# Performance work log

Measured on AMD Instinct MI355X. Metric: run time of the kernel, lower is better.

Reference implementation:

```python
import jax, jax.numpy as jnp
from jax import lax
import numpy as np

H = 51  # hidden size hardcoded in the module


def setup_inputs() -> dict:
    key = jax.random.key(0)
    ks = jax.random.split(key, 12)
    B, T = 4096, 256
    s_in = 1.0 / np.sqrt(H)
    inp = {
        "input": jax.random.normal(ks[0], (B, T), dtype=jnp.float32),
        # LSTMCell 1: input dim 1 -> hidden 51 (gates stacked i,f,g,o)
        "W_ih1": jax.random.uniform(ks[1], (4 * H, 1), jnp.float32, -s_in, s_in),
        "W_hh1": jax.random.uniform(ks[2], (4 * H, H), jnp.float32, -s_in, s_in),
        "b_ih1": jax.random.uniform(ks[3], (4 * H,), jnp.float32, -s_in, s_in),
        "b_hh1": jax.random.uniform(ks[4], (4 * H,), jnp.float32, -s_in, s_in),
        # LSTMCell 2: hidden 51 -> hidden 51
        "W_ih2": jax.random.uniform(ks[5], (4 * H, H), jnp.float32, -s_in, s_in),
        "W_hh2": jax.random.uniform(ks[6], (4 * H, H), jnp.float32, -s_in, s_in),
        "b_ih2": jax.random.uniform(ks[7], (4 * H,), jnp.float32, -s_in, s_in),
        "b_hh2": jax.random.uniform(ks[8], (4 * H,), jnp.float32, -s_in, s_in),
        # Linear head 51 -> 1
        "W_lin": jax.random.uniform(ks[9], (1, H), jnp.float32, -s_in, s_in),
        "b_lin": jax.random.uniform(ks[10], (1,), jnp.float32, -s_in, s_in),
    }
    return inp


def _lstm_cell(x_t, h, c, W_ih, W_hh, b_ih, b_hh):
    # PyTorch LSTMCell: gates = x W_ih^T + b_ih + h W_hh^T + b_hh, order i,f,g,o
    g = x_t @ W_ih.T + b_ih + h @ W_hh.T + b_hh  # [B, 4H]
    i, f, gg, o = jnp.split(g, 4, axis=-1)
    c_new = jax.nn.sigmoid(f) * c + jax.nn.sigmoid(i) * jnp.tanh(gg)
    h_new = jax.nn.sigmoid(o) * jnp.tanh(c_new)
    return h_new, c_new


def reference(input, W_ih1, W_hh1, b_ih1, b_hh1, W_ih2, W_hh2, b_ih2, b_hh2, W_lin, b_lin):
    B = input.shape[0]
    xs = input.T[:, :, None]  # [T, B, 1] -- one scalar feature per timestep

    def step(carry, x_t):
        h1, c1, h2, c2 = carry
        h1, c1 = _lstm_cell(x_t, h1, c1, W_ih1, W_hh1, b_ih1, b_hh1)
        h2, c2 = _lstm_cell(h1, h2, c2, W_ih2, W_hh2, b_ih2, b_hh2)
        out = h2 @ W_lin.T + b_lin  # [B, 1]
        return (h1, c1, h2, c2), out

    z = jnp.zeros((B, H), dtype=input.dtype)
    _, outs = lax.scan(step, (z, z, z, z), xs)  # outs: [T, B, 1]
    # torch.stack(outputs, 1).squeeze(2) -> [B, T]
    return outs[:, :, 0].T
```

## Files before the change

kernel.cpp:

```cpp
#include <hip/hip_runtime.h>

#define HH 51
#define TT 256
#define NB 16
#define L2E 1.442695041f

typedef __attribute__((ext_vector_type(8))) _Float16 half8;
typedef __attribute__((ext_vector_type(4))) float   floatx4;

#define MFMA16F(A,B,C) __builtin_amdgcn_mfma_f32_16x16x32_f16((A),(B),(C),0,0,0)

__device__ __forceinline__ float rcp_fast(float x) { return __builtin_amdgcn_rcpf(x); }
#if __has_builtin(__builtin_amdgcn_exp2f)
__device__ __forceinline__ float exp2_fast(float x) { return __builtin_amdgcn_exp2f(x); }
#else
__device__ __forceinline__ float exp2_fast(float x) { return __expf(0.69314718056f * x); }
#endif
__device__ __forceinline__ unsigned short f2h_bits(float v) {
    return __builtin_bit_cast(unsigned short, (_Float16)v);
}

__global__ void lstm_prep(const float* __restrict__ Whh1, const float* __restrict__ Wih1,
                          const float* __restrict__ bih1, const float* __restrict__ bhh1,
                          const float* __restrict__ Wih2, const float* __restrict__ Whh2,
                          const float* __restrict__ bih2, const float* __restrict__ bhh2,
                          const float* __restrict__ Wlin, const float* __restrict__ blin,
                          uint4* __restrict__ frags) {
    int tid = blockIdx.x * blockDim.x + threadIdx.x;
    if (tid >= 196 * 64) return;
    int f = tid >> 6, lane = tid & 63;
    int n = lane & 15, qq = lane >> 4;
    int hl, s, tau, cell;
    if (f < 64)       { cell = 1; int r = f;       hl = r & 1; r >>= 1; s = r & 1; tau = r >> 1; }
    else if (f < 192) { cell = 2; int r = f - 64;  hl = r & 1; r >>= 1; s = r & 3; tau = r >> 2; }
    else              { cell = 3; int r = f - 192; hl = r & 1; s = r >> 1; tau = 0; }
    int g = tau >> 2, U = tau & 3, u = U * 16 + n;
    float sc = (cell == 3) ? 1.0f : ((g == 2) ? 2.0f * L2E : L2E);
    unsigned int dw[4];
    for (int d = 0; d < 4; d++) {
        unsigned int packed = 0;
        for (int e = 0; e < 2; e++) {
            int jj = d * 2 + e;
            int k = s * 32 + qq * 8 + jj;
            float val = 0.f;
            if (cell == 1) {
                if (u < HH) {
                    if (k < HH)       val = Whh1[(g * HH + u) * HH + k];
                    else if (k == 51) val = bih1[g * HH + u] + bhh1[g * HH + u];
                    else              val = Wih1[g * HH + u];
                }
            } else if (cell == 2) {
                if (u < HH) {
                    if (k < 64) {
                        if (k < HH)       val = Wih2[(g * HH + u) * HH + k];
                        else if (k == 51) val = bih2[g * HH + u] + bhh2[g * HH + u];
                    } else {
                        int k2 = k - 64;
                        if (k2 < HH) val = Whh2[(g * HH + u) * HH + k2];
                    }
                }
            } else {
                if (n == 0) {
                    if (k < HH)       val = Wlin[k];
                    else if (k == 51) val = blin[0];
                }
            }
            val *= sc;
            _Float16 hi = (_Float16)val;
            unsigned short bits;
            if (hl) { float lo = val - (float)hi; bits = f2h_bits(lo); }
            else    { bits = __builtin_bit_cast(unsigned short, hi); }
            packed |= ((unsigned int)bits) << (16 * e);
        }
        dw[d] = packed;
    }
    frags[f * 64 + lane] = make_uint4(dw[0], dw[1], dw[2], dw[3]);
}

__launch_bounds__(512, 2)
__global__ void lstm_main(const float* __restrict__ input,
                          const uint4* __restrict__ frags,
                          float* __restrict__ out) {
    __shared__ __align__(16) unsigned int h1[2][16][36];
    __shared__ __align__(16) unsigned int h2[2][16][36];
    __shared__ __align__(16) float xb[(TT + 1) * 16];

    const int tid  = threadIdx.x;
    const int lane = tid & 63;
    const int w    = tid >> 6;
    const int l15  = lane & 15;
    const int q    = lane >> 4;
    const int b0g  = blockIdx.x * NB;
    const bool c2w = (w < 4);
    const int U    = c2w ? w : (w - 4);
    const int uc   = U * 16 + l15;
    const bool uok = (uc < HH);

    for (int i = tid; i < 2 * 16 * 36; i += 512) {
        ((unsigned*)h1)[i] = 0; ((unsigned*)h2)[i] = 0;
    }
    for (int c = 0; c < 2; c++) {
        int flat = tid + c * 512;
        int b = flat >> 6, t0 = (flat & 63) * 4;
        float4 v = *(const float4*)&input[(size_t)(b0g + b) * TT + t0];
        xb[(t0 + 0) * 16 + b] = v.x; xb[(t0 + 1) * 16 + b] = v.y;
        xb[(t0 + 2) * 16 + b] = v.z; xb[(t0 + 3) * 16 + b] = v.w;
    }
    if (tid < 16) xb[TT * 16 + tid] = 0.f;
    __syncthreads();
    if (tid < 16) {
        int b = tid;
        int wi51 = ((25 + 4 * (b >> 1)) & 31) * 2 + 1;
        int wi52 = ((26 + 4 * (b >> 1)) & 31) * 2 + 0;
        int wi53 = ((26 + 4 * (b >> 1)) & 31) * 2 + 1;
        ((unsigned short*)&h1[1][b][0])[wi51] = 0x3C00;
        float x0 = input[(size_t)(b0g + b) * TT];
        _Float16 xh = (_Float16)x0;
        ((unsigned short*)&h1[1][b][0])[wi52] = __builtin_bit_cast(unsigned short, xh);
        ((unsigned short*)&h1[1][b][0])[wi53] = f2h_bits(x0 - (float)xh);
    }

    half8 fr[32];
    if (c2w) {
#pragma unroll
        for (int g = 0; g < 4; g++) {
            int tau = g * 4 + U;
#pragma unroll
            for (int s = 0; s < 4; s++) {
                fr[g * 8 + s * 2 + 0] = __builtin_bit_cast(half8, frags[(64 + (tau * 4 + s) * 2 + 0) * 64 + lane]);
                fr[g * 8 + s * 2 + 1] = __builtin_bit_cast(half8, frags[(64 + (tau * 4 + s) * 2 + 1) * 64 + lane]);
            }
        }
    } else {
#pragma unroll
        for (int g = 0; g < 4; g++) {
            int tau = g * 4 + U;
#pragma unroll
            for (int s = 0; s < 2; s++) {
                fr[g * 4 + s * 2 + 0] = __builtin_bit_cast(half8, frags[((tau * 2 + s) * 2 + 0) * 64 + lane]);
                fr[g * 4 + s * 2 + 1] = __builtin_bit_cast(half8, frags[((tau * 2 + s) * 2 + 1) * 64 + lane]);
            }
        }
#pragma unroll
        for (int s = 0; s < 2; s++) {
            fr[16 + s * 2 + 0] = __builtin_bit_cast(half8, frags[(192 + s * 2 + 0) * 64 + lane]);
            fr[16 + s * 2 + 1] = __builtin_bit_cast(half8, frags[(192 + s * 2 + 1) * 64 + lane]);
        }
    }
    floatx4 zacc = {0.f, 0.f, 0.f, 0.f};
    float cst[4] = {0.f, 0.f, 0.f, 0.f};
    const int baseA = (q * 4 + 4 * (l15 >> 1)) & 31;
    const int baseB = (baseA + 16) & 31;

    __syncthreads();

#define GTAIL(DG, FG, SGN)                                                      \
    _Pragma("unroll")                                                           \
    for (int r = 0; r < 4; r++) {                                               \
        float e = exp2_fast(SGN (DG)[r]);                                       \
        (FG)[r] = rcp_fast(1.0f + e);                                           \
    }

#define STEP(IT, P)                                                             \
    do {                                                                        \
        if (c2w) {                                                              \
            if ((IT) >= 1 && (IT) <= TT) {               \
                half8 a0 = *(const half8*)&h1[1 - (P)][l15][baseA];             \
                half8 a1 = *(const half8*)&h1[1 - (P)][l15][baseB];             \
                half8 a2 = *(const half8*)&h2[(P)][l15][baseA];                 \
                half8 a3 = *(const half8*)&h2[(P)][l15][baseB];                 \
                floatx4 d0, d1, d2, d3;                                         \
                d0 = MFMA16F(a0, fr[0],  zacc); d0 = MFMA16F(a0, fr[1],  d0);   \
                d1 = MFMA16F(a0, fr[8],  zacc); d1 = MFMA16F(a0, fr[9],  d1);   \
                d2 = MFMA16F(a0, fr[16], zacc); d2 = MFMA16F(a0, fr[17], d2);   \
                d3 = MFMA16F(a0, fr[24], zacc); d3 = MFMA16F(a0, fr[25], d3);   \
                d0 = MFMA16F(a1, fr[2],  d0);   d0 = MFMA16F(a1, fr[3],  d0);   \
                d1 = MFMA16F(a1, fr[10], d1);   d1 = MFMA16F(a1, fr[11], d1);   \
                d2 = MFMA16F(a1, fr[18], d2);   d2 = MFMA16F(a1, fr[19], d2);   \
                d3 = MFMA16F(a1, fr[26], d3);   d3 = MFMA16F(a1, fr[27], d3);   \
                d0 = MFMA16F(a2, fr[4],  d0);   d0 = MFMA16F(a2, fr[5],  d0);   \
                d1 = MFMA16F(a2, fr[12], d1);   d1 = MFMA16F(a2, fr[13], d1);   \
                d2 = MFMA16F(a2, fr[20], d2);   d2 = MFMA16F(a2, fr[21], d2);   \
                d3 = MFMA16F(a2, fr[28], d3);   d3 = MFMA16F(a2, fr[29], d3);   \
                d0 = MFMA16F(a3, fr[6],  d0);   d0 = MFMA16F(a3, fr[7],  d0);   \
                d1 = MFMA16F(a3, fr[14], d1);   d1 = MFMA16F(a3, fr[15], d1);   \
                d2 = MFMA16F(a3, fr[22], d2);   d2 = MFMA16F(a3, fr[23], d2);   \
                d3 = MFMA16F(a3, fr[30], d3);   d3 = MFMA16F(a3, fr[31], d3);   \
                floatx4 f0, f1, f2, f3;                                         \
                GTAIL(d0, f0, -) GTAIL(d1, f1, -) GTAIL(d2, f2, +) GTAIL(d3, f3, -) \
                _Pragma("unroll")                                               \
                for (int r = 0; r < 4; r++) {                                   \
                    float tgs = fmaf(-4.0f * L2E, f2[r], 2.0f * L2E);           \
                    float cn  = fmaf(f1[r], cst[r], f0[r] * tgs);               \
                    cst[r] = cn;                                                \
                    float th = fmaf(-2.0f, rcp_fast(1.0f + exp2_fast(cn)), 1.0f); \
                    float hv = f3[r] * th;                                      \
                    hv = uok ? hv : (uc == 51 ? 1.0f : 0.f);                    \
                    int bb = q * 4 + r;                                         \
                    int wi = (((uc >> 1) + 4 * (bb >> 1)) & 31) * 2 + (uc & 1); \
                    ((unsigned short*)&h2[1 - (P)][bb][0])[wi] = f2h_bits(hv);  \
                }                                                               \
            }                                                                   \
        } else {                                                                \
            if ((IT) <= TT - 1) {                          \
                float4 xn = {0.f, 0.f, 0.f, 0.f};                               \
                if (uc >= HH) xn = *(const float4*)&xb[((IT) + 1) * 16 + q * 4]; \
                half8 a0 = *(const half8*)&h1[1 - (P)][l15][baseA];             \
                half8 a1 = *(const half8*)&h1[1 - (P)][l15][baseB];             \
                floatx4 d0, d1, d2, d3;                                         \
                d0 = MFMA16F(a0, fr[0],  zacc); d0 = MFMA16F(a0, fr[1],  d0);   \
                d1 = MFMA16F(a0, fr[4],  zacc); d1 = MFMA16F(a0, fr[5],  d1);   \
                d2 = MFMA16F(a0, fr[8],  zacc); d2 = MFMA16F(a0, fr[9],  d2);   \
                d3 = MFMA16F(a0, fr[12], zacc); d3 = MFMA16F(a0, fr[13], d3);   \
                d0 = MFMA16F(a1, fr[2],  d0);   d0 = MFMA16F(a1, fr[3],  d0);   \
                d1 = MFMA16F(a1, fr[6],  d1);   d1 = MFMA16F(a1, fr[7],  d1);   \
                d2 = MFMA16F(a1, fr[10], d2);   d2 = MFMA16F(a1, fr[11], d2);   \
                d3 = MFMA16F(a1, fr[14], d3);   d3 = MFMA16F(a1, fr[15], d3);   \
                floatx4 f0, f1, f2, f3;                                         \
                GTAIL(d0, f0, -) GTAIL(d1, f1, -) GTAIL(d2, f2, +) GTAIL(d3, f3, -) \
                _Pragma("unroll")                                               \
                for (int r = 0; r < 4; r++) {                                   \
                    float tgs = fmaf(-4.0f * L2E, f2[r], 2.0f * L2E);           \
                    float cn  = fmaf(f1[r], cst[r], f0[r] * tgs);               \
                    cst[r] = cn;                                                \
                    float th = fmaf(-2.0f, rcp_fast(1.0f + exp2_fast(cn)), 1.0f); \
                    float hv = f3[r] * th;                                      \
                    hv = uok ? hv                                               \
                             : (uc == 51 ? 1.0f                                 \
                             : (uc == 52 ? xn[r]                                \
                             : (uc == 53 ? xn[r] - (float)(_Float16)xn[r] : 0.f))); \
                    int bb = q * 4 + r;                                         \
                    int wi = (((uc >> 1) + 4 * (bb >> 1)) & 31) * 2 + (uc & 1); \
                    ((unsigned short*)&h1[(P)][bb][0])[wi] = f2h_bits(hv);      \
                }                                                               \
            }                                                                   \
            if ((IT) >= 2 && (w - 4) == ((IT) & 3)) {         \
                half8 a2 = *(const half8*)&h2[(P)][l15][baseA];                 \
                half8 a3 = *(const half8*)&h2[(P)][l15][baseB];                 \
                floatx4 ho;                                                     \
                ho = MFMA16F(a2, fr[16], zacc); ho = MFMA16F(a2, fr[17], ho);   \
                ho = MFMA16F(a3, fr[18], ho);   ho = MFMA16F(a3, fr[19], ho);   \
                if (l15 == 0) {                                                 \
                    _Pragma("unroll")                                           \
                    for (int r = 0; r < 4; r++)                                 \
                        out[(size_t)(b0g + q * 4 + r) * TT + ((IT) - 2)] = ho[r]; \
                }                                                               \
            }                                                                   \
        }                                                                       \
        __syncthreads();                                                        \
    } while (0)

    for (int itp = 0; itp < TT + 2; itp += 2) {
        STEP(itp, 0);
        STEP(itp + 1, 1);
    }
#undef STEP
#undef GTAIL
}

extern "C" void kernel_launch(void* const* d_in, const int* in_sizes, int n_in,
                              void* d_out, int out_size, void* d_ws, size_t ws_size,
                              hipStream_t stream) {
    const float* input = (const float*)d_in[0];
    const float* Wih1  = (const float*)d_in[1];
    const float* Whh1  = (const float*)d_in[2];
    const float* bih1  = (const float*)d_in[3];
    const float* bhh1  = (const float*)d_in[4];
    const float* Wih2  = (const float*)d_in[5];
    const float* Whh2  = (const float*)d_in[6];
    const float* bih2  = (const float*)d_in[7];
    const float* bhh2  = (const float*)d_in[8];
    const float* Wlin  = (const float*)d_in[9];
    const float* blin  = (const float*)d_in[10];

    uint4* frags = (uint4*)d_ws;
    int B = in_sizes[0] / TT;

    lstm_prep<<<49, 256, 0, stream>>>(Whh1, Wih1, bih1, bhh1, Wih2, Whh2,
                                      bih2, bhh2, Wlin, blin, frags);
    lstm_main<<<B / NB, 512, 0, stream>>>(input, frags, (float*)d_out);
}
```

Before: 377.2 us.

## Merge both LSTM cells into each wave and halve batch per block

Each wave now computes both layer-1 and layer-2 gates for its hidden-unit slice, instead of splitting the cells across separate 4-wave groups. Blocks drop to 256 threads and 8 batch rows, so twice as many blocks launch. The linear-head fragments are reloaded from global memory on each output step instead of being held in registers. The intent is to cut per-block wave count and spread work over more blocks. In exchange, the two cells now run one after the other inside each wave, half of each 16-row MFMA tile is idle, and register pressure rises from holding both weight sets.

```diff
diff --git a/kernel.cpp b/kernel.cpp
--- a/kernel.cpp
+++ b/kernel.cpp
@@ -2,7 +2,7 @@
 
 #define HH 51
 #define TT 256
-#define NB 16
+#define NB 8
 #define L2E 1.442695041f
 
 typedef __attribute__((ext_vector_type(8))) _Float16 half8;
@@ -77,13 +77,13 @@
     frags[f * 64 + lane] = make_uint4(dw[0], dw[1], dw[2], dw[3]);
 }
 
-__launch_bounds__(512, 2)
+__launch_bounds__(256, 2)
 __global__ void lstm_main(const float* __restrict__ input,
                           const uint4* __restrict__ frags,
                           float* __restrict__ out) {
     __shared__ __align__(16) unsigned int h1[2][16][36];
     __shared__ __align__(16) unsigned int h2[2][16][36];
-    __shared__ __align__(16) float xb[(TT + 1) * 16];
+    __shared__ __align__(16) float xb[(TT + 1) * NB];
 
     const int tid  = threadIdx.x;
     const int lane = tid & 63;
@@ -91,24 +91,22 @@
     const int l15  = lane & 15;
     const int q    = lane >> 4;
     const int b0g  = blockIdx.x * NB;
-    const bool c2w = (w < 4);
-    const int U    = c2w ? w : (w - 4);
-    const int uc   = U * 16 + l15;
+    const int uc   = w * 16 + l15;
     const bool uok = (uc < HH);
 
-    for (int i = tid; i < 2 * 16 * 36; i += 512) {
+    for (int i = tid; i < 2 * 16 * 36; i += 256) {
         ((unsigned*)h1)[i] = 0; ((unsigned*)h2)[i] = 0;
     }
     for (int c = 0; c < 2; c++) {
-        int flat = tid + c * 512;
+        int flat = tid + c * 256;
         int b = flat >> 6, t0 = (flat & 63) * 4;
         float4 v = *(const float4*)&input[(size_t)(b0g + b) * TT + t0];
-        xb[(t0 + 0) * 16 + b] = v.x; xb[(t0 + 1) * 16 + b] = v.y;
-        xb[(t0 + 2) * 16 + b] = v.z; xb[(t0 + 3) * 16 + b] = v.w;
-    }
-    if (tid < 16) xb[TT * 16 + tid] = 0.f;
+        xb[(t0 + 0) * NB + b] = v.x; xb[(t0 + 1) * NB + b] = v.y;
+        xb[(t0 + 2) * NB + b] = v.z; xb[(t0 + 3) * NB + b] = v.w;
+    }
+    if (tid < NB) xb[TT * NB + tid] = 0.f;
     __syncthreads();
-    if (tid < 16) {
+    if (tid < NB) {
         int b = tid;
         int wi51 = ((25 + 4 * (b >> 1)) & 31) * 2 + 1;
         int wi52 = ((26 + 4 * (b >> 1)) & 31) * 2 + 0;
@@ -120,35 +118,24 @@
         ((unsigned short*)&h1[1][b][0])[wi53] = f2h_bits(x0 - (float)xh);
     }
 
-    half8 fr[32];
-    if (c2w) {
+    half8 fr1[16], fr2[32];
 #pragma unroll
-        for (int g = 0; g < 4; g++) {
-            int tau = g * 4 + U;
+    for (int g = 0; g < 4; g++) {
+        int tau = g * 4 + w;
 #pragma unroll
-            for (int s = 0; s < 4; s++) {
-                fr[g * 8 + s * 2 + 0] = __builtin_bit_cast(half8, frags[(64 + (tau * 4 + s) * 2 + 0) * 64 + lane]);
-                fr[g * 8 + s * 2 + 1] = __builtin_bit_cast(half8, frags[(64 + (tau * 4 + s) * 2 + 1) * 64 + lane]);
-            }
-        }
-    } else {
-#pragma unroll
-        for (int g = 0; g < 4; g++) {
-            int tau = g * 4 + U;
-#pragma unroll
-            for (int s = 0; s < 2; s++) {
-                fr[g * 4 + s * 2 + 0] = __builtin_bit_cast(half8, frags[((tau * 2 + s) * 2 + 0) * 64 + lane]);
-                fr[g * 4 + s * 2 + 1] = __builtin_bit_cast(half8, frags[((tau * 2 + s) * 2 + 1) * 64 + lane]);
-            }
+        for (int s = 0; s < 2; s++) {
+            fr1[g * 4 + s * 2 + 0] = __builtin_bit_cast(half8, frags[((tau * 2 + s) * 2 + 0) * 64 + lane]);
+            fr1[g * 4 + s * 2 + 1] = __builtin_bit_cast(half8, frags[((tau * 2 + s) * 2 + 1) * 64 + lane]);
         }
 #pragma unroll
-        for (int s = 0; s < 2; s++) {
-            fr[16 + s * 2 + 0] = __builtin_bit_cast(half8, frags[(192 + s * 2 + 0) * 64 + lane]);
-            fr[16 + s * 2 + 1] = __builtin_bit_cast(half8, frags[(192 + s * 2 + 1) * 64 + lane]);
+        for (int s = 0; s < 4; s++) {
+            fr2[g * 8 + s * 2 + 0] = __builtin_bit_cast(half8, frags[(64 + (tau * 4 + s) * 2 + 0) * 64 + lane]);
+            fr2[g * 8 + s * 2 + 1] = __builtin_bit_cast(half8, frags[(64 + (tau * 4 + s) * 2 + 1) * 64 + lane]);
         }
     }
     floatx4 zacc = {0.f, 0.f, 0.f, 0.f};
-    float cst[4] = {0.f, 0.f, 0.f, 0.f};
+    float cst1[4] = {0.f, 0.f, 0.f, 0.f};
+    float cst2[4] = {0.f, 0.f, 0.f, 0.f};
     const int baseA = (q * 4 + 4 * (l15 >> 1)) & 31;
     const int baseB = (baseA + 16) & 31;
 
@@ -163,87 +150,91 @@
 
 #define STEP(IT, P)                                                             \
     do {                                                                        \
-        if (c2w) {                                                              \
-            if ((IT) >= 1 && (IT) <= TT) {               \
-                half8 a0 = *(const half8*)&h1[1 - (P)][l15][baseA];             \
-                half8 a1 = *(const half8*)&h1[1 - (P)][l15][baseB];             \
-                half8 a2 = *(const half8*)&h2[(P)][l15][baseA];                 \
-                half8 a3 = *(const half8*)&h2[(P)][l15][baseB];                 \
-                floatx4 d0, d1, d2, d3;                                         \
-                d0 = MFMA16F(a0, fr[0],  zacc); d0 = MFMA16F(a0, fr[1],  d0);   \
-                d1 = MFMA16F(a0, fr[8],  zacc); d1 = MFMA16F(a0, fr[9],  d1);   \
-                d2 = MFMA16F(a0, fr[16], zacc); d2 = MFMA16F(a0, fr[17], d2);   \
-                d3 = MFMA16F(a0, fr[24], zacc); d3 = MFMA16F(a0, fr[25], d3);   \
-                d0 = MFMA16F(a1, fr[2],  d0);   d0 = MFMA16F(a1, fr[3],  d0);   \
-                d1 = MFMA16F(a1, fr[10], d1);   d1 = MFMA16F(a1, fr[11], d1);   \
-                d2 = MFMA16F(a1, fr[18], d2);   d2 = MFMA16F(a1, fr[19], d2);   \
-                d3 = MFMA16F(a1, fr[26], d3);   d3 = MFMA16F(a1, fr[27], d3);   \
-                d0 = MFMA16F(a2, fr[4],  d0);   d0 = MFMA16F(a2, fr[5],  d0);   \
-                d1 = MFMA16F(a2, fr[12], d1);   d1 = MFMA16F(a2, fr[13], d1);   \
-                d2 = MFMA16F(a2, fr[20], d2);   d2 = MFMA16F(a2, fr[21], d2);   \
-                d3 = MFMA16F(a2, fr[28], d3);   d3 = MFMA16F(a2, fr[29], d3);   \
-                d0 = MFMA16F(a3, fr[6],  d0);   d0 = MFMA16F(a3, fr[7],  d0);   \
-                d1 = MFMA16F(a3, fr[14], d1);   d1 = MFMA16F(a3, fr[15], d1);   \
-                d2 = MFMA16F(a3, fr[22], d2);   d2 = MFMA16F(a3, fr[23], d2);   \
-                d3 = MFMA16F(a3, fr[30], d3);   d3 = MFMA16F(a3, fr[31], d3);   \
-                floatx4 f0, f1, f2, f3;                                         \
-                GTAIL(d0, f0, -) GTAIL(d1, f1, -) GTAIL(d2, f2, +) GTAIL(d3, f3, -) \
+        half8 a0 = *(const half8*)&h1[1 - (P)][l15][baseA];       \
+        half8 a1 = *(const half8*)&h1[1 - (P)][l15][baseB];                     \
+        half8 a2 = *(const half8*)&h2[(P)][l15][baseA];           \
+        half8 a3 = *(const half8*)&h2[(P)][l15][baseB];                         \
+          \
+        if ((IT) >= 2 && (((IT) & 3) == w)) {                                   \
+            half8 hf0 = __builtin_bit_cast(half8, frags[(192 + 0) * 64 + lane]);\
+            half8 hf1 = __builtin_bit_cast(half8, frags[(192 + 1) * 64 + lane]);\
+            half8 hf2 = __builtin_bit_cast(half8, frags[(192 + 2) * 64 + lane]);\
+            half8 hf3 = __builtin_bit_cast(half8, frags[(192 + 3) * 64 + lane]);\
+            floatx4 ho;                                                         \
+            ho = MFMA16F(a2, hf0, zacc); ho = MFMA16F(a2, hf1, ho);             \
+            ho = MFMA16F(a3, hf2, ho);   ho = MFMA16F(a3, hf3, ho);             \
+            if (l15 == 0 && q < 2) {                                            \
                 _Pragma("unroll")                                               \
-                for (int r = 0; r < 4; r++) {                                   \
-                    float tgs = fmaf(-4.0f * L2E, f2[r], 2.0f * L2E);           \
-                    float cn  = fmaf(f1[r], cst[r], f0[r] * tgs);               \
-                    cst[r] = cn;                                                \
-                    float th = fmaf(-2.0f, rcp_fast(1.0f + exp2_fast(cn)), 1.0f); \
-                    float hv = f3[r] * th;                                      \
-                    hv = uok ? hv : (uc == 51 ? 1.0f : 0.f);                    \
-                    int bb = q * 4 + r;                                         \
-                    int wi = (((uc >> 1) + 4 * (bb >> 1)) & 31) * 2 + (uc & 1); \
-                    ((unsigned short*)&h2[1 - (P)][bb][0])[wi] = f2h_bits(hv);  \
-                }                                                               \
+                for (int r = 0; r < 4; r++)                                     \
+                    out[(size_t)(b0g + q * 4 + r) * TT + ((IT) - 2)] = ho[r];   \
             }                                                                   \
-        } else {                                                                \
-            if ((IT) <= TT - 1) {                          \
-                float4 xn = {0.f, 0.f, 0.f, 0.f};                               \
-                if (uc >= HH) xn = *(const float4*)&xb[((IT) + 1) * 16 + q * 4]; \
-                half8 a0 = *(const half8*)&h1[1 - (P)][l15][baseA];             \
-                half8 a1 = *(const half8*)&h1[1 - (P)][l15][baseB];             \
-                floatx4 d0, d1, d2, d3;                                         \
-                d0 = MFMA16F(a0, fr[0],  zacc); d0 = MFMA16F(a0, fr[1],  d0);   \
-                d1 = MFMA16F(a0, fr[4],  zacc); d1 = MFMA16F(a0, fr[5],  d1);   \
-                d2 = MFMA16F(a0, fr[8],  zacc); d2 = MFMA16F(a0, fr[9],  d2);   \
-                d3 = MFMA16F(a0, fr[12], zacc); d3 = MFMA16F(a0, fr[13], d3);   \
-                d0 = MFMA16F(a1, fr[2],  d0);   d0 = MFMA16F(a1, fr[3],  d0);   \
-                d1 = MFMA16F(a1, fr[6],  d1);   d1 = MFMA16F(a1, fr[7],  d1);   \
-                d2 = MFMA16F(a1, fr[10], d2);   d2 = MFMA16F(a1, fr[11], d2);   \
-                d3 = MFMA16F(a1, fr[14], d3);   d3 = MFMA16F(a1, fr[15], d3);   \
-                floatx4 f0, f1, f2, f3;                                         \
-                GTAIL(d0, f0, -) GTAIL(d1, f1, -) GTAIL(d2, f2, +) GTAIL(d3, f3, -) \
-                _Pragma("unroll")                                               \
-                for (int r = 0; r < 4; r++) {                                   \
-                    float tgs = fmaf(-4.0f * L2E, f2[r], 2.0f * L2E);           \
-                    float cn  = fmaf(f1[r], cst[r], f0[r] * tgs);               \
-                    cst[r] = cn;                                                \
-                    float th = fmaf(-2.0f, rcp_fast(1.0f + exp2_fast(cn)), 1.0f); \
-                    float hv = f3[r] * th;                                      \
-                    hv = uok ? hv                                               \
-                             : (uc == 51 ? 1.0f                                 \
-                             : (uc == 52 ? xn[r]                                \
-                             : (uc == 53 ? xn[r] - (float)(_Float16)xn[r] : 0.f))); \
-                    int bb = q * 4 + r;                                         \
+        }                                                                       \
+          \
+        if ((IT) <= TT - 1) {                                                   \
+            float4 xn = {0.f, 0.f, 0.f, 0.f};                                   \
+            if (uc >= HH && q < 2) xn = *(const float4*)&xb[((IT) + 1) * NB + q * 4]; \
+            floatx4 d0, d1, d2, d3;                                             \
+            d0 = MFMA16F(a0, fr1[0],  zacc); d0 = MFMA16F(a0, fr1[1],  d0);     \
+            d1 = MFMA16F(a0, fr1[4],  zacc); d1 = MFMA16F(a0, fr1[5],  d1);     \
+            d2 = MFMA16F(a0, fr1[8],  zacc); d2 = MFMA16F(a0, fr1[9],  d2);     \
+            d3 = MFMA16F(a0, fr1[12], zacc); d3 = MFMA16F(a0, fr1[13], d3);     \
+            d0 = MFMA16F(a1, fr1[2],  d0);   d0 = MFMA16F(a1, fr1[3],  d0);     \
+            d1 = MFMA16F(a1, fr1[6],  d1);   d1 = MFMA16F(a1, fr1[7],  d1);     \
+            d2 = MFMA16F(a1, fr1[10], d2);   d2 = MFMA16F(a1, fr1[11], d2);     \
+            d3 = MFMA16F(a1, fr1[14], d3);   d3 = MFMA16F(a1, fr1[15], d3);     \
+            floatx4 f0, f1, f2, f3;                                             \
+            GTAIL(d0, f0, -) GTAIL(d1, f1, -) GTAIL(d2, f2, +) GTAIL(d3, f3, -) \
+            _Pragma("unroll")                                                   \
+            for (int r = 0; r < 4; r++) {                                       \
+                float tgs = fmaf(-4.0f * L2E, f2[r], 2.0f * L2E);               \
+                float cn  = fmaf(f1[r], cst1[r], f0[r] * tgs);                  \
+                cst1[r] = cn;                                                   \
+                float th = fmaf(-2.0f, rcp_fast(1.0f + exp2_fast(cn)), 1.0f);   \
+                float hv = f3[r] * th;                                          \
+                hv = uok ? hv                                                   \
+                         : (uc == 51 ? 1.0f                                     \
+                         : (uc == 52 ? xn[r]                                    \
+                         : (uc == 53 ? xn[r] - (float)(_Float16)xn[r] : 0.f))); \
+                int bb = q * 4 + r;                                             \
+                if (bb < NB) {                                                  \
                     int wi = (((uc >> 1) + 4 * (bb >> 1)) & 31) * 2 + (uc & 1); \
                     ((unsigned short*)&h1[(P)][bb][0])[wi] = f2h_bits(hv);      \
                 }                                                               \
             }                                                                   \
-            if ((IT) >= 2 && (w - 4) == ((IT) & 3)) {         \
-                half8 a2 = *(const half8*)&h2[(P)][l15][baseA];                 \
-                half8 a3 = *(const half8*)&h2[(P)][l15][baseB];                 \
-                floatx4 ho;                                                     \
-                ho = MFMA16F(a2, fr[16], zacc); ho = MFMA16F(a2, fr[17], ho);   \
-                ho = MFMA16F(a3, fr[18], ho);   ho = MFMA16F(a3, fr[19], ho);   \
-                if (l15 == 0) {                                                 \
-                    _Pragma("unroll")                                           \
-                    for (int r = 0; r < 4; r++)                                 \
-                        out[(size_t)(b0g + q * 4 + r) * TT + ((IT) - 2)] = ho[r]; \
+        }                                                                       \
+          \
+        if ((IT) >= 1 && (IT) <= TT) {                                          \
+            floatx4 e0, e1, e2, e3;                                             \
+            e0 = MFMA16F(a0, fr2[0],  zacc); e0 = MFMA16F(a0, fr2[1],  e0);     \
+            e1 = MFMA16F(a0, fr2[8],  zacc); e1 = MFMA16F(a0, fr2[9],  e1);     \
+            e2 = MFMA16F(a0, fr2[16], zacc); e2 = MFMA16F(a0, fr2[17], e2);     \
+            e3 = MFMA16F(a0, fr2[24], zacc); e3 = MFMA16F(a0, fr2[25], e3);     \
+            e0 = MFMA16F(a1, fr2[2],  e0);   e0 = MFMA16F(a1, fr2[3],  e0);     \
+            e1 = MFMA16F(a1, fr2[10], e1);   e1 = MFMA16F(a1, fr2[11], e1);     \
+            e2 = MFMA16F(a1, fr2[18], e2);   e2 = MFMA16F(a1, fr2[19], e2);     \
+            e3 = MFMA16F(a1, fr2[26], e3);   e3 = MFMA16F(a1, fr2[27], e3);     \
+            e0 = MFMA16F(a2, fr2[4],  e0);   e0 = MFMA16F(a2, fr2[5],  e0);     \
+            e1 = MFMA16F(a2, fr2[12], e1);   e1 = MFMA16F(a2, fr2[13], e1);     \
+            e2 = MFMA16F(a2, fr2[20], e2);   e2 = MFMA16F(a2, fr2[21], e2);     \
+            e3 = MFMA16F(a2, fr2[28], e3);   e3 = MFMA16F(a2, fr2[29], e3);     \
+            e0 = MFMA16F(a3, fr2[6],  e0);   e0 = MFMA16F(a3, fr2[7],  e0);     \
+            e1 = MFMA16F(a3, fr2[14], e1);   e1 = MFMA16F(a3, fr2[15], e1);     \
+            e2 = MFMA16F(a3, fr2[22], e2);   e2 = MFMA16F(a3, fr2[23], e2);     \
+            e3 = MFMA16F(a3, fr2[30], e3);   e3 = MFMA16F(a3, fr2[31], e3);     \
+            floatx4 f0, f1, f2, f3;                                             \
+            GTAIL(e0, f0, -) GTAIL(e1, f1, -) GTAIL(e2, f2, +) GTAIL(e3, f3, -) \
+            _Pragma("unroll")                                                   \
+            for (int r = 0; r < 4; r++) {                                       \
+                float tgs = fmaf(-4.0f * L2E, f2[r], 2.0f * L2E);               \
+                float cn  = fmaf(f1[r], cst2[r], f0[r] * tgs);                  \
+                cst2[r] = cn;                                                   \
+                float th = fmaf(-2.0f, rcp_fast(1.0f + exp2_fast(cn)), 1.0f);   \
+                float hv = f3[r] * th;                                          \
+                hv = uok ? hv : (uc == 51 ? 1.0f : 0.f);                        \
+                int bb = q * 4 + r;                                             \
+                if (bb < NB) {                                                  \
+                    int wi = (((uc >> 1) + 4 * (bb >> 1)) & 31) * 2 + (uc & 1); \
+                    ((unsigned short*)&h2[1 - (P)][bb][0])[wi] = f2h_bits(hv);  \
                 }                                                               \
             }                                                                   \
         }                                                                       \
@@ -278,5 +269,5 @@
 
     lstm_prep<<<49, 256, 0, stream>>>(Whh1, Wih1, bih1, bhh1, Wih2, Whh2,
                                       bih2, bhh2, Wlin, blin, frags);
-    lstm_main<<<B / NB, 512, 0, stream>>>(input, frags, (float*)d_out);
-}
+    lstm_main<<<B / NB, 256, 0, stream>>>(input, frags, (float*)d_out);
+}
```

Result: slower. 650.0 us (+72.3%).
